# Kernel tuning notes

Hardware: AMD Instinct MI355X
Metric: run time of the kernel (lower is better)

Reference implementation:

```python
import jax, jax.numpy as jnp
import numpy as np

B, T, C = 4, 2048, 1024
T_REF = 512
H = 16
D = C // H


def setup_inputs() -> dict:
    key = jax.random.key(0)
    ks = jax.random.split(key, 16)
    s = 0.02
    return {
        "x": jax.random.normal(ks[0], (B, T, C), jnp.float32),
        "ref_feat": jax.random.normal(ks[1], (B, T_REF, C), jnp.float32),
        "Wq": jax.random.normal(ks[2], (C, C), jnp.float32) * s,
        "bq": jax.random.normal(ks[3], (C,), jnp.float32) * s,
        "Wk": jax.random.normal(ks[4], (C, C), jnp.float32) * s,
        "bk": jax.random.normal(ks[5], (C,), jnp.float32) * s,
        "Wv": jax.random.normal(ks[6], (C, C), jnp.float32) * s,
        "bv": jax.random.normal(ks[7], (C,), jnp.float32) * s,
        "Wrk": jax.random.normal(ks[8], (C, C), jnp.float32) * s,
        "brk": jax.random.normal(ks[9], (C,), jnp.float32) * s,
        "Wrv": jax.random.normal(ks[10], (C, C), jnp.float32) * s,
        "brv": jax.random.normal(ks[11], (C,), jnp.float32) * s,
        "Wp": jax.random.normal(ks[12], (C, C), jnp.float32) * s,
        "bp": jax.random.normal(ks[13], (C,), jnp.float32) * s,
    }


def _heads(y):
    # [B, T, C] -> [B, H, T, D]
    b, t, c = y.shape
    return y.reshape(b, t, H, D).transpose(0, 2, 1, 3)


def reference(x, ref_feat, Wq, bq, Wk, bk, Wv, bv, Wrk, brk, Wrv, brv, Wp, bp):
    b, t, c = x.shape
    t_ref = ref_feat.shape[1]
    q = _heads(x @ Wq + bq)                      # [B,H,T,D]
    k = _heads(x @ Wk + bk)                      # [B,H,T,D]
    v = _heads(x @ Wv + bv)
    ref_k = _heads(ref_feat @ Wrk + brk)         # [B,H,Tref,D]
    ref_v = _heads(ref_feat @ Wrv + brv)
    k = jnp.concatenate([k, ref_k], axis=2)      # [B,H,T+Tref,D]
    v = jnp.concatenate([v, ref_v], axis=2)

    # additive bias: causal over self keys, fully visible over ref keys
    causal = jnp.tril(jnp.ones((t, t), dtype=bool))
    full_mask = jnp.concatenate([causal, jnp.ones((t, t_ref), dtype=bool)], axis=1)
    bias = jnp.where(full_mask, 0.0, -jnp.inf).astype(x.dtype)  # [T, T+Tref]

    scale = 1.0 / jnp.sqrt(jnp.asarray(D, x.dtype))
    scores = jnp.einsum("bhtd,bhsd->bhts", q, k) * scale + bias
    attn = jax.nn.softmax(scores, axis=-1)
    y = jnp.einsum("bhts,bhsd->bhtd", attn, v)   # [B,H,T,D]
    y = y.transpose(0, 2, 1, 3).reshape(b, t, c)
    return y @ Wp + bp
```

## Files before the change

kernel.cpp:

```cpp
#include <hip/hip_runtime.h>
#include <hip/hip_bf16.h>

typedef short s16x4 __attribute__((ext_vector_type(4)));
typedef short s16x8 __attribute__((ext_vector_type(8)));
typedef __bf16 bf16x8 __attribute__((ext_vector_type(8)));
typedef float f32x4 __attribute__((ext_vector_type(4)));

#define DEVI static __device__ __forceinline__
#define QSCALE 0.18033688011112042f

DEVI unsigned short f2bf(float x) {
  union { float f; unsigned u; } a; a.f = x;
  unsigned r = a.u + 0x7fffu + ((a.u >> 16) & 1u);
  return (unsigned short)(r >> 16);
}
DEVI bf16x8 asbf(s16x8 v) {
  union { s16x8 s; bf16x8 b; } u; u.s = v; return u.b;
}
DEVI unsigned cvtpk(float lo, float hi) {
  unsigned r;
  asm("v_cvt_pk_bf16_f32 %0, %1, %2" : "=v"(r) : "v"(lo), "v"(hi));
  return r;
}
DEVI void gload16(const void* g, void* l) {
  __builtin_amdgcn_global_load_lds(
      (const __attribute__((address_space(1))) void*)g,
      (__attribute__((address_space(3))) void*)l, 16, 0, 0);
}

struct PrepArgs {
  const float* x; const float* ref; unsigned short* xg;
  const float* w[6]; unsigned short* o[6];
};

__global__ __launch_bounds__(256)
void prep(PrepArgs a) {
  __shared__ short tile[64][65];
  const int bid = blockIdx.x, t = threadIdx.x;
  if (bid < 5120) {
    int f = bid * 256 + t;
    int row = f >> 7, c8 = f & 127;
    const float* src = (row < 8192 ? a.x + (size_t)row * 1024
                                   : a.ref + (size_t)(row - 8192) * 1024) + c8 * 8;
    float4 v0 = *(const float4*)src;
    float4 v1 = *(const float4*)(src + 4);
    s16x8 o;
    o[0] = (short)f2bf(v0.x); o[1] = (short)f2bf(v0.y);
    o[2] = (short)f2bf(v0.z); o[3] = (short)f2bf(v0.w);
    o[4] = (short)f2bf(v1.x); o[5] = (short)f2bf(v1.y);
    o[6] = (short)f2bf(v1.z); o[7] = (short)f2bf(v1.w);
    int cs = (c8 & ~7) | ((c8 ^ row) & 7);
    *(s16x8*)(a.xg + (size_t)row * 1024 + cs * 8) = o;
  } else {
    int q = bid - 5120;
    int z = q >> 8, b2 = q & 255;
    const float* __restrict__ W = a.w[z];
    unsigned short* __restrict__ WT = a.o[z];
    const float sc = (z == 0) ? QSCALE : 1.0f;
    const int n0 = (b2 & 15) * 64;
    const int k0 = (b2 >> 4) * 64;
#pragma unroll
    for (int i = 0; i < 4; i++) {
      int f = t + i * 256;
      int r = f >> 4, c = (f & 15) * 4;
      float4 v = *(const float4*)(W + (size_t)(k0 + r) * 1024 + n0 + c);
      tile[r][c + 0] = (short)f2bf(v.x * sc);
      tile[r][c + 1] = (short)f2bf(v.y * sc);
      tile[r][c + 2] = (short)f2bf(v.z * sc);
      tile[r][c + 3] = (short)f2bf(v.w * sc);
    }
    __syncthreads();
#pragma unroll
    for (int i = 0; i < 2; i++) {
      int f = t + i * 256;
      int r = f >> 3, c8 = f & 7;
      s16x8 o;
#pragma unroll
      for (int j = 0; j < 8; j++) o[j] = tile[c8 * 8 + j][r];
      *(s16x8*)(WT + (size_t)(n0 + r) * 1024 + k0 + ((c8 ^ (r & 7)) & 7) * 8) = o;
    }
  }
}

template<int MODE>
__global__ __launch_bounds__(256, 3)
void gemm_bt(const unsigned short* __restrict__ A, const unsigned short* __restrict__ BT,
             const float* __restrict__ b0, const float* __restrict__ b1,
             const float* __restrict__ b2,
             void* __restrict__ o0, void* __restrict__ o1, void* __restrict__ o2)
{
  const int K = 1024;
  __shared__ __align__(16) short As[128][64];
  __shared__ __align__(16) short Bs[128][64];
  const int t = threadIdx.x;
  const int lane = t & 63, wid = t >> 6;
  const int wm = wid >> 1, wn = wid & 1;
  const int lr = lane & 15, lg = lane >> 4;
  const size_t m0 = (size_t)blockIdx.y * 128;
  const int n0 = blockIdx.x * 128;

  f32x4 acc[4][4];
#pragma unroll
  for (int i = 0; i < 4; i++)
#pragma unroll
    for (int j = 0; j < 4; j++) acc[i][j] = (f32x4){0.f, 0.f, 0.f, 0.f};

  const unsigned short* Abase = A + m0 * K;
  const unsigned short* Bbase = BT + (size_t)n0 * K;
  const int r_ld = t >> 3, cb_ld = t & 7;

  for (int k0 = 0; k0 < K; k0 += 64) {
#pragma unroll
    for (int i = 0; i < 4; i++) {
      int r = r_ld + i * 32;
      gload16(Abase + (size_t)r * K + k0 + cb_ld * 8,
              (short*)As + (i * 256 + wid * 64) * 8);
      gload16(Bbase + (size_t)r * K + k0 + cb_ld * 8,
              (short*)Bs + (i * 256 + wid * 64) * 8);
    }
    __syncthreads();
#pragma unroll
    for (int ks = 0; ks < 2; ks++) {
      s16x8 af[4], bfr[4];
#pragma unroll
      for (int i = 0; i < 4; i++)
        af[i] = *(const s16x8*)&As[wm * 64 + i * 16 + lr][(((ks * 4 + lg) ^ lr) & 7) * 8];
#pragma unroll
      for (int i = 0; i < 4; i++)
        bfr[i] = *(const s16x8*)&Bs[wn * 64 + i * 16 + lr][(((ks * 4 + lg) ^ lr) & 7) * 8];
#pragma unroll
      for (int mi = 0; mi < 4; mi++)
#pragma unroll
        for (int ni = 0; ni < 4; ni++)
          acc[mi][ni] = __builtin_amdgcn_mfma_f32_16x16x32_bf16(
              asbf(af[mi]), asbf(bfr[ni]), acc[mi][ni], 0, 0, 0);
    }
    __syncthreads();
  }

  const int seg = n0 >> 10;
  const float* bb = (seg == 0) ? b0 : (seg == 1 ? b1 : b2);
#pragma unroll
  for (int mi = 0; mi < 4; mi++) {
#pragma unroll
    for (int ni = 0; ni < 4; ni++) {
      int cg = n0 + wn * 64 + ni * 16 + lr;
      int c = cg & 1023;
      float bv = bb[c];
      if (MODE == 0 && seg == 0) bv *= QSCALE;
      const bool vseg = (MODE == 0 && seg == 2) || (MODE == 1 && seg == 1);
      if (MODE != 2 && vseg) {
        int rm0 = (int)m0 + wm * 64 + mi * 16 + lg * 4;
        int d = c & 63, hh = c >> 6;
        int bb_, s;
        if (MODE == 0) { bb_ = rm0 >> 11; s = rm0 & 2047; }
        else           { bb_ = rm0 >> 9;  s = 2048 + (rm0 & 511); }
        int scol = (s & ~63) + ((((s >> 3) ^ d) & 7) << 3) + (s & 7);
        unsigned short* dst = (unsigned short*)(MODE == 0 ? o2 : o1);
        short4 pk4;
        pk4.x = (short)f2bf(acc[mi][ni][0] + bv);
        pk4.y = (short)f2bf(acc[mi][ni][1] + bv);
        pk4.z = (short)f2bf(acc[mi][ni][2] + bv);
        pk4.w = (short)f2bf(acc[mi][ni][3] + bv);
        *(short4*)(dst + ((size_t)(bb_ * 16 + hh) * 64 + d) * 2560 + scol) = pk4;
      } else {
#pragma unroll
        for (int r = 0; r < 4; r++) {
          int rm = (int)m0 + wm * 64 + mi * 16 + lg * 4 + r;
          float val = acc[mi][ni][r] + bv;
          if (MODE == 2) {
            ((float*)o0)[(size_t)rm * 1024 + cg] = val;
          } else {
            size_t orow; unsigned short* dst; bool swz;
            if (MODE == 0) {
              if (seg == 0) { dst = (unsigned short*)o0; orow = rm; swz = false; }
              else { orow = (size_t)(rm >> 11) * 2560 + (rm & 2047);
                     dst = (unsigned short*)o1; swz = true; }
            } else {
              orow = (size_t)(rm >> 9) * 2560 + 2048 + (rm & 511);
              dst = (unsigned short*)o0; swz = true;
            }
            int cc = c;
            if (swz) cc = (c & ~63) | ((((c >> 3) ^ (int)orow) & 7) << 3) | (c & 7);
            dst[orow * 1024 + cc] = f2bf(val);
          }
        }
      }
    }
  }
}

__global__ __launch_bounds__(256, 4)
void attn(const unsigned short* __restrict__ Q, const unsigned short* __restrict__ Kb,
          const unsigned short* __restrict__ VbT, unsigned short* __restrict__ Y)
{
  const int T = 2048, S = 2560, C = 1024, TREF = 512;
  __shared__ __align__(16) short Ks[2][64][64];
  __shared__ __align__(16) short Vt[2][64][64];
  const int t = threadIdx.x;
  const int lane = t & 63, wid = t >> 6;
  const int lr = lane & 15, lg = lane >> 4;

  const int bid = blockIdx.x;
  const int xcd = bid & 7, idx = bid >> 3;
  const int bh = xcd * 8 + (idx >> 4);
  const int bx = idx & 15;
  const int b = bh >> 4;
  const int hc = (bh & 15) * 64;
  const int qt[2] = {bx, 31 - bx};

  s16x8 qf[2][2];
#pragma unroll
  for (int j = 0; j < 2; j++) {
    size_t qrow = (size_t)(b * T + qt[j] * 64 + wid * 16 + lr);
#pragma unroll
    for (int ks = 0; ks < 2; ks++)
      qf[j][ks] = *(const s16x8*)(Q + qrow * C + hc + ks * 32 + lg * 8);
  }

  float mrow[2] = {-1e30f, -1e30f}, lsum[2] = {0.f, 0.f};
  f32x4 o[2][4];
#pragma unroll
  for (int j = 0; j < 2; j++)
#pragma unroll
    for (int d = 0; d < 4; d++) o[j][d] = (f32x4){0.f, 0.f, 0.f, 0.f};

  const int nself = 32 - bx;
  const int ntiles = nself + TREF / 64;

  auto s0_of = [&](int ti2) {
    return (ti2 < nself) ? ti2 * 64 : T + (ti2 - nself) * 64;
  };
  const int r_ld = t >> 3, cb_ld = t & 7;
  auto load_K = [&](int ti2, int buf) {
    int s0 = s0_of(ti2);
    const unsigned short* Krow = Kb + (size_t)(b * S + s0) * C + hc;
#pragma unroll
    for (int i = 0; i < 2; i++)
      gload16(Krow + (size_t)(r_ld + i * 32) * C + cb_ld * 8,
              (short*)&Ks[buf][0][0] + (i * 256 + wid * 64) * 8);
  };
  auto load_V = [&](int ti2, int buf) {
    int s0 = s0_of(ti2);
    const unsigned short* Vr = VbT + (size_t)bh * 64 * S + s0;
#pragma unroll
    for (int i = 0; i < 2; i++)
      gload16(Vr + (size_t)(r_ld + i * 32) * S + cb_ld * 8,
              (short*)&Vt[buf][0][0] + (i * 256 + wid * 64) * 8);
  };

  load_K(0, 0);
  load_V(0, 0);
  __syncthreads();

  for (int ti = 0; ti < ntiles; ti++) {
    const int cur = ti & 1;
    const bool more = (ti + 1 < ntiles);
    if (more) { load_K(ti + 1, cur ^ 1); load_V(ti + 1, cur ^ 1); }

    const bool a0 = (ti <= bx) || (ti >= nself);

    f32x4 sa[2][4];
#pragma unroll
    for (int j = 0; j < 2; j++)
#pragma unroll
      for (int nt = 0; nt < 4; nt++) sa[j][nt] = (f32x4){0.f, 0.f, 0.f, 0.f};
    __builtin_amdgcn_s_setprio(1);
#pragma unroll
    for (int ks = 0; ks < 2; ks++) {
      s16x8 kf[4];
#pragma unroll
      for (int nt = 0; nt < 4; nt++)
        kf[nt] = *(const s16x8*)&Ks[cur][nt * 16 + lr][(((ks * 4 + lg) ^ lr) & 7) * 8];
#pragma unroll
      for (int nt = 0; nt < 4; nt++) {
        if (a0)
          sa[0][nt] = __builtin_amdgcn_mfma_f32_16x16x32_bf16(
              asbf(kf[nt]), asbf(qf[0][ks]), sa[0][nt], 0, 0, 0);
        sa[1][nt] = __builtin_amdgcn_mfma_f32_16x16x32_bf16(
            asbf(kf[nt]), asbf(qf[1][ks]), sa[1][nt], 0, 0, 0);
      }
    }
    __builtin_amdgcn_s_setprio(0);

    s16x8 pa[2][2];
#pragma unroll
    for (int j = 0; j < 2; j++) {
      if (j == 0 && !a0) continue;

      if (ti == (j == 0 ? bx : nself - 1)) {
        int qg = wid * 16 + lr;
#pragma unroll
        for (int nt = 0; nt < 4; nt++)
#pragma unroll
          for (int r = 0; r < 4; r++)
            if (nt * 16 + lg * 4 + r > qg) sa[j][nt][r] = -1e30f;
      }

      float mm[4];
#pragma unroll
      for (int nt = 0; nt < 4; nt++)
        mm[nt] = fmaxf(fmaxf(sa[j][nt][0], sa[j][nt][1]),
                       fmaxf(sa[j][nt][2], sa[j][nt][3]));
      float lm = fmaxf(fmaxf(mm[0], mm[1]), fmaxf(mm[2], mm[3]));

      if (!__all(lm <= mrow[j] + 8.f)) {
        float tm = lm;
        tm = fmaxf(tm, __shfl_xor(tm, 16, 64));
        tm = fmaxf(tm, __shfl_xor(tm, 32, 64));
        float mn = fmaxf(mrow[j], tm);
        float alpha = __builtin_amdgcn_exp2f(mrow[j] - mn);
        mrow[j] = mn;
        lsum[j] *= alpha;
#pragma unroll
        for (int r = 0; r < 4; r++) {
          float ar = __shfl(alpha, lg * 4 + r, 64);
#pragma unroll
          for (int dt = 0; dt < 4; dt++) o[j][dt][r] *= ar;
        }
      }

      unsigned pk2[4][2];
      float rsn[4];
#pragma unroll
      for (int nt = 0; nt < 4; nt++) {
        float p0 = __builtin_amdgcn_exp2f(sa[j][nt][0] - mrow[j]);
        float p1 = __builtin_amdgcn_exp2f(sa[j][nt][1] - mrow[j]);
        float p2 = __builtin_amdgcn_exp2f(sa[j][nt][2] - mrow[j]);
        float p3 = __builtin_amdgcn_exp2f(sa[j][nt][3] - mrow[j]);
        rsn[nt] = (p0 + p1) + (p2 + p3);
        pk2[nt][0] = cvtpk(p0, p1);
        pk2[nt][1] = cvtpk(p2, p3);
      }
      lsum[j] += (rsn[0] + rsn[1]) + (rsn[2] + rsn[3]);

#pragma unroll
      for (int ks = 0; ks < 2; ks++) {
        union { unsigned w[4]; s16x8 v; } U;
#pragma unroll
        for (int w = 0; w < 4; w++) {
          int srcL = lr + (((lg & 1) * 2 + (w >> 1)) << 4);
          unsigned v0 = __shfl((int)pk2[2 * ks][w & 1], srcL, 64);
          unsigned v1 = __shfl((int)pk2[2 * ks + 1][w & 1], srcL, 64);
          U.w[w] = (lg & 2) ? v1 : v0;
        }
        pa[j][ks] = U.v;
      }
    }

    __builtin_amdgcn_s_setprio(1);
#pragma unroll
    for (int ks = 0; ks < 2; ks++) {
      s16x8 vf[4];
#pragma unroll
      for (int dt = 0; dt < 4; dt++)
        vf[dt] = *(const s16x8*)&Vt[cur][dt * 16 + lr][(((ks * 4 + lg) ^ lr) & 7) * 8];
#pragma unroll
      for (int dt = 0; dt < 4; dt++) {
        if (a0)
          o[0][dt] = __builtin_amdgcn_mfma_f32_16x16x32_bf16(
              asbf(pa[0][ks]), asbf(vf[dt]), o[0][dt], 0, 0, 0);
        o[1][dt] = __builtin_amdgcn_mfma_f32_16x16x32_bf16(
            asbf(pa[1][ks]), asbf(vf[dt]), o[1][dt], 0, 0, 0);
      }
    }
    __builtin_amdgcn_s_setprio(0);

    __syncthreads();
  }

#pragma unroll
  for (int j = 0; j < 2; j++) {
    float tot = lsum[j];
    tot += __shfl_xor(tot, 16, 64);
    tot += __shfl_xor(tot, 32, 64);
#pragma unroll
    for (int r = 0; r < 4; r++) {
      float inv = 1.0f / __shfl(tot, lg * 4 + r, 64);
      int qrow = b * T + qt[j] * 64 + wid * 16 + lg * 4 + r;
#pragma unroll
      for (int dt = 0; dt < 4; dt++) {
        int col = hc + dt * 16 + lr;
        int cb = col >> 3;
        int cs = (cb & ~7) | ((cb ^ qrow) & 7);
        Y[(size_t)qrow * C + cs * 8 + (col & 7)] = f2bf(o[j][dt][r] * inv);
      }
    }
  }
}

extern "C" void kernel_launch(void* const* d_in, const int* in_sizes, int n_in,
                              void* d_out, int out_size, void* d_ws, size_t ws_size,
                              hipStream_t stream) {
  const float* x   = (const float*)d_in[0];
  const float* ref = (const float*)d_in[1];
  const float* Wq  = (const float*)d_in[2];
  const float* bq  = (const float*)d_in[3];
  const float* Wk  = (const float*)d_in[4];
  const float* bk  = (const float*)d_in[5];
  const float* Wv  = (const float*)d_in[6];
  const float* bv  = (const float*)d_in[7];
  const float* Wrk = (const float*)d_in[8];
  const float* brk = (const float*)d_in[9];
  const float* Wrv = (const float*)d_in[10];
  const float* brv = (const float*)d_in[11];
  const float* Wp  = (const float*)d_in[12];
  const float* bp  = (const float*)d_in[13];
  float* out = (float*)d_out;

  char* ws = (char*)d_ws;
  auto alloc = [&](size_t bytes) {
    char* p = ws; ws += (bytes + 255) & ~(size_t)255; return p;
  };
  const size_t WB = (size_t)1024 * 1024 * 2;
  unsigned short* Wall = (unsigned short*)alloc(5 * WB);
  unsigned short* WpT  = (unsigned short*)alloc(WB);
  unsigned short* xg  = (unsigned short*)alloc((size_t)10240 * 1024 * 2);
  unsigned short* rg  = xg + (size_t)8192 * 1024;
  unsigned short* qb  = (unsigned short*)alloc((size_t)8192 * 1024 * 2);
  unsigned short* kb  = (unsigned short*)alloc((size_t)4 * 2560 * 1024 * 2);
  unsigned short* vbT = (unsigned short*)alloc((size_t)4096 * 2560 * 2);
  unsigned short* yb  = (unsigned short*)alloc((size_t)8192 * 1024 * 2);

  dim3 tb(256);

  PrepArgs pa;
  pa.x = x; pa.ref = ref; pa.xg = xg;
  pa.w[0] = Wq;  pa.o[0] = Wall;
  pa.w[1] = Wk;  pa.o[1] = Wall + (size_t)1024 * 1024;
  pa.w[2] = Wv;  pa.o[2] = Wall + (size_t)2048 * 1024;
  pa.w[3] = Wrk; pa.o[3] = Wall + (size_t)3072 * 1024;
  pa.w[4] = Wrv; pa.o[4] = Wall + (size_t)4096 * 1024;
  pa.w[5] = Wp;  pa.o[5] = WpT;
  prep<<<dim3(6656), tb, 0, stream>>>(pa);

  gemm_bt<0><<<dim3(24, 64), tb, 0, stream>>>(xg, Wall, bq, bk, bv, qb, kb, vbT);
  gemm_bt<1><<<dim3(16, 16), tb, 0, stream>>>(rg, Wall + (size_t)3072 * 1024,
                                              brk, brv, nullptr, kb, vbT, nullptr);

  attn<<<dim3(1024), tb, 0, stream>>>(qb, kb, vbT, yb);

  gemm_bt<2><<<dim3(8, 64), tb, 0, stream>>>(yb, WpT, bp, bp, bp, out, out, out);
}
```

Baseline: 224.6 us.

## Split paired causal query tiles into one tile per block, heaviest first

The attention kernel stops pairing query tile bx with tile 31-bx in one block and gives each block a single 64-row query tile, launching twice as many blocks. Blocks are ordered so the longest causal tiles are scheduled first, and launch bounds are raised to allow five blocks per CU now that per-thread state is halved. The aim is more parallelism, higher occupancy and less register pressure. In exchange, each K/V tile loaded into shared memory now feeds only one query tile, so global and LDS traffic per unit of work roughly doubles, and tail balance now depends on the heaviest-first ordering.

```diff
diff --git a/kernel.cpp b/kernel.cpp
--- a/kernel.cpp
+++ b/kernel.cpp
@@ -190,7 +190,7 @@
   }
 }
 
-__global__ __launch_bounds__(256, 4)
+__global__ __launch_bounds__(256, 5)
 void attn(const unsigned short* __restrict__ Q, const unsigned short* __restrict__ Kb,
           const unsigned short* __restrict__ VbT, unsigned short* __restrict__ Y)
 {
@@ -203,29 +203,27 @@
 
   const int bid = blockIdx.x;
   const int xcd = bid & 7, idx = bid >> 3;
-  const int bh = xcd * 8 + (idx >> 4);
-  const int bx = idx & 15;
+  const int g = idx & 7;
+  const int bx = 31 - (idx >> 3);
+  const int bh = xcd * 8 + g;
   const int b = bh >> 4;
   const int hc = (bh & 15) * 64;
-  const int qt[2] = {bx, 31 - bx};
-
-  s16x8 qf[2][2];
-#pragma unroll
-  for (int j = 0; j < 2; j++) {
-    size_t qrow = (size_t)(b * T + qt[j] * 64 + wid * 16 + lr);
+  const int q0 = bx * 64;
+
+  s16x8 qf[2];
+  {
+    size_t qrow = (size_t)(b * T + q0 + wid * 16 + lr);
 #pragma unroll
     for (int ks = 0; ks < 2; ks++)
-      qf[j][ks] = *(const s16x8*)(Q + qrow * C + hc + ks * 32 + lg * 8);
-  }
-
-  float mrow[2] = {-1e30f, -1e30f}, lsum[2] = {0.f, 0.f};
-  f32x4 o[2][4];
-#pragma unroll
-  for (int j = 0; j < 2; j++)
-#pragma unroll
-    for (int d = 0; d < 4; d++) o[j][d] = (f32x4){0.f, 0.f, 0.f, 0.f};
-
-  const int nself = 32 - bx;
+      qf[ks] = *(const s16x8*)(Q + qrow * C + hc + ks * 32 + lg * 8);
+  }
+
+  float mrow = -1e30f, lsum = 0.f;
+  f32x4 o[4];
+#pragma unroll
+  for (int d = 0; d < 4; d++) o[d] = (f32x4){0.f, 0.f, 0.f, 0.f};
+
+  const int nself = bx + 1;
   const int ntiles = nself + TREF / 64;
 
   auto s0_of = [&](int ti2) {
@@ -258,13 +256,9 @@
     const bool more = (ti + 1 < ntiles);
     if (more) { load_K(ti + 1, cur ^ 1); load_V(ti + 1, cur ^ 1); }
 
-    const bool a0 = (ti <= bx) || (ti >= nself);
-
-    f32x4 sa[2][4];
-#pragma unroll
-    for (int j = 0; j < 2; j++)
-#pragma unroll
-      for (int nt = 0; nt < 4; nt++) sa[j][nt] = (f32x4){0.f, 0.f, 0.f, 0.f};
+    f32x4 sa[4];
+#pragma unroll
+    for (int nt = 0; nt < 4; nt++) sa[nt] = (f32x4){0.f, 0.f, 0.f, 0.f};
     __builtin_amdgcn_s_setprio(1);
 #pragma unroll
     for (int ks = 0; ks < 2; ks++) {
@@ -273,79 +267,69 @@
       for (int nt = 0; nt < 4; nt++)
         kf[nt] = *(const s16x8*)&Ks[cur][nt * 16 + lr][(((ks * 4 + lg) ^ lr) & 7) * 8];
 #pragma unroll
-      for (int nt = 0; nt < 4; nt++) {
-        if (a0)
-          sa[0][nt] = __builtin_amdgcn_mfma_f32_16x16x32_bf16(
-              asbf(kf[nt]), asbf(qf[0][ks]), sa[0][nt], 0, 0, 0);
-        sa[1][nt] = __builtin_amdgcn_mfma_f32_16x16x32_bf16(
-            asbf(kf[nt]), asbf(qf[1][ks]), sa[1][nt], 0, 0, 0);
+      for (int nt = 0; nt < 4; nt++)
+        sa[nt] = __builtin_amdgcn_mfma_f32_16x16x32_bf16(
+            asbf(kf[nt]), asbf(qf[ks]), sa[nt], 0, 0, 0);
+    }
+    __builtin_amdgcn_s_setprio(0);
+
+    if (ti == bx) {
+      int qg = wid * 16 + lr;
+#pragma unroll
+      for (int nt = 0; nt < 4; nt++)
+#pragma unroll
+        for (int r = 0; r < 4; r++)
+          if (nt * 16 + lg * 4 + r > qg) sa[nt][r] = -1e30f;
+    }
+
+    float mm[4];
+#pragma unroll
+    for (int nt = 0; nt < 4; nt++)
+      mm[nt] = fmaxf(fmaxf(sa[nt][0], sa[nt][1]), fmaxf(sa[nt][2], sa[nt][3]));
+    float lm = fmaxf(fmaxf(mm[0], mm[1]), fmaxf(mm[2], mm[3]));
+
+    if (!__all(lm <= mrow + 8.f)) {
+      float tm = lm;
+      tm = fmaxf(tm, __shfl_xor(tm, 16, 64));
+      tm = fmaxf(tm, __shfl_xor(tm, 32, 64));
+      float mn = fmaxf(mrow, tm);
+      float alpha = __builtin_amdgcn_exp2f(mrow - mn);
+      mrow = mn;
+      lsum *= alpha;
+#pragma unroll
+      for (int r = 0; r < 4; r++) {
+        float ar = __shfl(alpha, lg * 4 + r, 64);
+#pragma unroll
+        for (int dt = 0; dt < 4; dt++) o[dt][r] *= ar;
       }
     }
-    __builtin_amdgcn_s_setprio(0);
-
-    s16x8 pa[2][2];
-#pragma unroll
-    for (int j = 0; j < 2; j++) {
-      if (j == 0 && !a0) continue;
-
-      if (ti == (j == 0 ? bx : nself - 1)) {
-        int qg = wid * 16 + lr;
-#pragma unroll
-        for (int nt = 0; nt < 4; nt++)
-#pragma unroll
-          for (int r = 0; r < 4; r++)
-            if (nt * 16 + lg * 4 + r > qg) sa[j][nt][r] = -1e30f;
+
+    unsigned pk2[4][2];
+    float rsn[4];
+#pragma unroll
+    for (int nt = 0; nt < 4; nt++) {
+      float p0 = __builtin_amdgcn_exp2f(sa[nt][0] - mrow);
+      float p1 = __builtin_amdgcn_exp2f(sa[nt][1] - mrow);
+      float p2 = __builtin_amdgcn_exp2f(sa[nt][2] - mrow);
+      float p3 = __builtin_amdgcn_exp2f(sa[nt][3] - mrow);
+      rsn[nt] = (p0 + p1) + (p2 + p3);
+      pk2[nt][0] = cvtpk(p0, p1);
+      pk2[nt][1] = cvtpk(p2, p3);
+    }
+    lsum += (rsn[0] + rsn[1]) + (rsn[2] + rsn[3]);
+
+    s16x8 pa[2];
+#pragma unroll
+    for (int ks = 0; ks < 2; ks++) {
+      union { unsigned w[4]; s16x8 v; } U;
+#pragma unroll
+      for (int w = 0; w < 4; w++) {
+        int srcL = lr + (((lg & 1) * 2 + (w >> 1)) << 4);
+        unsigned v0 = __shfl((int)pk2[2 * ks][w & 1], srcL, 64);
+        unsigned v1 = __shfl((int)pk2[2 * ks + 1][w & 1], srcL, 64);
+        U.w[w] = (lg & 2) ? v1 : v0;
       }
-
-      float mm[4];
-#pragma unroll
-      for (int nt = 0; nt < 4; nt++)
-        mm[nt] = fmaxf(fmaxf(sa[j][nt][0], sa[j][nt][1]),
-                       fmaxf(sa[j][nt][2], sa[j][nt][3]));
-      float lm = fmaxf(fmaxf(mm[0], mm[1]), fmaxf(mm[2], mm[3]));
-
-      if (!__all(lm <= mrow[j] + 8.f)) {
-        float tm = lm;
-        tm = fmaxf(tm, __shfl_xor(tm, 16, 64));
-        tm = fmaxf(tm, __shfl_xor(tm, 32, 64));
-        float mn = fmaxf(mrow[j], tm);
-        float alpha = __builtin_amdgcn_exp2f(mrow[j] - mn);
-        mrow[j] = mn;
-        lsum[j] *= alpha;
-#pragma unroll
-        for (int r = 0; r < 4; r++) {
-          float ar = __shfl(alpha, lg * 4 + r, 64);
-#pragma unroll
-          for (int dt = 0; dt < 4; dt++) o[j][dt][r] *= ar;
-        }
-      }
-
-      unsigned pk2[4][2];
-      float rsn[4];
-#pragma unroll
-      for (int nt = 0; nt < 4; nt++) {
-        float p0 = __builtin_amdgcn_exp2f(sa[j][nt][0] - mrow[j]);
-        float p1 = __builtin_amdgcn_exp2f(sa[j][nt][1] - mrow[j]);
-        float p2 = __builtin_amdgcn_exp2f(sa[j][nt][2] - mrow[j]);
-        float p3 = __builtin_amdgcn_exp2f(sa[j][nt][3] - mrow[j]);
-        rsn[nt] = (p0 + p1) + (p2 + p3);
-        pk2[nt][0] = cvtpk(p0, p1);
-        pk2[nt][1] = cvtpk(p2, p3);
-      }
-      lsum[j] += (rsn[0] + rsn[1]) + (rsn[2] + rsn[3]);
-
-#pragma unroll
-      for (int ks = 0; ks < 2; ks++) {
-        union { unsigned w[4]; s16x8 v; } U;
-#pragma unroll
-        for (int w = 0; w < 4; w++) {
-          int srcL = lr + (((lg & 1) * 2 + (w >> 1)) << 4);
-          unsigned v0 = __shfl((int)pk2[2 * ks][w & 1], srcL, 64);
-          unsigned v1 = __shfl((int)pk2[2 * ks + 1][w & 1], srcL, 64);
-          U.w[w] = (lg & 2) ? v1 : v0;
-        }
-        pa[j][ks] = U.v;
-      }
+      pa[ks] = U.v;
     }
 
     __builtin_amdgcn_s_setprio(1);
@@ -356,35 +340,28 @@
       for (int dt = 0; dt < 4; dt++)
         vf[dt] = *(const s16x8*)&Vt[cur][dt * 16 + lr][(((ks * 4 + lg) ^ lr) & 7) * 8];
 #pragma unroll
-      for (int dt = 0; dt < 4; dt++) {
-        if (a0)
-          o[0][dt] = __builtin_amdgcn_mfma_f32_16x16x32_bf16(
-              asbf(pa[0][ks]), asbf(vf[dt]), o[0][dt], 0, 0, 0);
-        o[1][dt] = __builtin_amdgcn_mfma_f32_16x16x32_bf16(
-            asbf(pa[1][ks]), asbf(vf[dt]), o[1][dt], 0, 0, 0);
-      }
+      for (int dt = 0; dt < 4; dt++)
+        o[dt] = __builtin_amdgcn_mfma_f32_16x16x32_bf16(
+            asbf(pa[ks]), asbf(vf[dt]), o[dt], 0, 0, 0);
     }
     __builtin_amdgcn_s_setprio(0);
 
     __syncthreads();
   }
 
-#pragma unroll
-  for (int j = 0; j < 2; j++) {
-    float tot = lsum[j];
-    tot += __shfl_xor(tot, 16, 64);
-    tot += __shfl_xor(tot, 32, 64);
-#pragma unroll
-    for (int r = 0; r < 4; r++) {
-      float inv = 1.0f / __shfl(tot, lg * 4 + r, 64);
-      int qrow = b * T + qt[j] * 64 + wid * 16 + lg * 4 + r;
-#pragma unroll
-      for (int dt = 0; dt < 4; dt++) {
-        int col = hc + dt * 16 + lr;
-        int cb = col >> 3;
-        int cs = (cb & ~7) | ((cb ^ qrow) & 7);
-        Y[(size_t)qrow * C + cs * 8 + (col & 7)] = f2bf(o[j][dt][r] * inv);
-      }
+  float tot = lsum;
+  tot += __shfl_xor(tot, 16, 64);
+  tot += __shfl_xor(tot, 32, 64);
+#pragma unroll
+  for (int r = 0; r < 4; r++) {
+    float inv = 1.0f / __shfl(tot, lg * 4 + r, 64);
+    int qrow = b * T + q0 + wid * 16 + lg * 4 + r;
+#pragma unroll
+    for (int dt = 0; dt < 4; dt++) {
+      int col = hc + dt * 16 + lr;
+      int cb = col >> 3;
+      int cs = (cb & ~7) | ((cb ^ qrow) & 7);
+      Y[(size_t)qrow * C + cs * 8 + (col & 7)] = f2bf(o[dt][r] * inv);
     }
   }
 }
@@ -438,7 +415,7 @@
   gemm_bt<1><<<dim3(16, 16), tb, 0, stream>>>(rg, Wall + (size_t)3072 * 1024,
                                               brk, brv, nullptr, kb, vbT, nullptr);
 
-  attn<<<dim3(1024), tb, 0, stream>>>(qb, kb, vbT, yb);
+  attn<<<dim3(2048), tb, 0, stream>>>(qb, kb, vbT, yb);
 
   gemm_bt<2><<<dim3(8, 64), tb, 0, stream>>>(yb, WpT, bp, bp, bp, out, out, out);
 }
```

Measured after the change: 222.0 us. No clear change (-1.2%).
